# Kernel tuning notes

Hardware: AMD Instinct MI355X
Metric: run time of the kernel (lower is better)

The kernel has to match this reference:

```python
import jax, jax.numpy as jnp
import numpy as np


def _conv1x1(x, w, b):
    # x: (B,Ci,H,W), w: (Co,Ci) -> (B,Co,H,W)
    return jnp.einsum('bchw,oc->bohw', x, w) + b[None, :, None, None]


def _conv3x3(x, w, b):
    # x: (B,Ci,H,W), w: (Co,Ci,3,3), stride 1, padding 1 ('SAME')
    y = jax.lax.conv_general_dilated(
        x, w, window_strides=(1, 1), padding='SAME',
        dimension_numbers=('NCHW', 'OIHW', 'NCHW'))
    return y + b[None, :, None, None]


def setup_inputs() -> dict:
    key = jax.random.key(0)
    ks = jax.random.split(key, 10)
    N, B, Cc, Cf, H, W = 3, 8, 128, 256, 64, 64
    s = 0.05  # weight scale to keep attention logits well-conditioned
    return {
        'contexts': jax.random.normal(ks[0], (N, B, Cc, 2 * H, 2 * W), jnp.float32),
        'mainstream': jax.random.normal(ks[1], (B, Cf, H, W), jnp.float32),
        'Wc_w': jax.random.normal(ks[2], (Cc, Cc), jnp.float32) * s,
        'Wc_b': jax.random.normal(ks[3], (Cc,), jnp.float32) * s,
        'Wf_w': jax.random.normal(ks[4], (Cc, Cf), jnp.float32) * s,
        'Wf_b': jax.random.normal(ks[5], (Cc,), jnp.float32) * s,
        'Wk_w': jax.random.normal(ks[6], (Cc, Cf), jnp.float32) * s,
        'Wk_b': jax.random.normal(ks[7], (Cc,), jnp.float32) * s,
        'Wv_w': jax.random.normal(ks[8], (Cc, Cf, 3, 3), jnp.float32) * s,
        'Wv_b': jax.random.normal(ks[9], (Cc,), jnp.float32) * s,
    }


def reference(contexts, mainstream, Wc_w, Wc_b, Wf_w, Wf_b, Wk_w, Wk_b, Wv_w, Wv_b):
    N, B, Cc = contexts.shape[0], contexts.shape[1], contexts.shape[2]
    H, W = mainstream.shape[2], mainstream.shape[3]

    q = _conv1x1(mainstream, Wf_w, Wf_b)        # (B,Cc,H,W) queries
    mkey = _conv1x1(mainstream, Wk_w, Wk_b)     # (B,Cc,H,W) mainline keys
    vals = _conv3x3(mainstream, Wv_w, Wv_b)     # (B,Cc,H,W) mainline values
    ckeys = jax.vmap(lambda c: _conv1x1(c, Wc_w, Wc_b))(contexts)  # (N,B,Cc,2H,2W)

    # unfold 2x2 sub-pixel blocks: (.., 2H, 2W) -> (.., H, 2, W, 2)
    ckeys = ckeys.reshape(N, B, Cc, H, 2, W, 2)
    cfeat = contexts.reshape(N, B, Cc, H, 2, W, 2)

    # per-pixel cross-attention logits: context keys . query
    logits_ctx = jnp.einsum('nbchiwj,bchw->nbhiwj', ckeys, q)      # (N,B,H,2,W,2)
    # mainline key . query (same logit for all 4 sub-pixels)
    logit_main = jnp.einsum('bchw,bchw->bhw', mkey, q)[None, :, :, None, :, None]
    logits = jnp.concatenate(
        [logits_ctx, jnp.broadcast_to(logit_main, (1, B, H, 2, W, 2))], axis=0)

    attn = jax.nn.softmax(logits, axis=0)                          # (N+1,B,H,2,W,2)

    vfeat = jnp.broadcast_to(vals[None, :, :, :, None, :, None],
                             (1, B, Cc, H, 2, W, 2))
    feats = jnp.concatenate([cfeat, vfeat], axis=0)                # (N+1,B,Cc,H,2,W,2)

    out = jnp.einsum('nbhiwj,nbchiwj->bchiwj', attn, feats)        # (B,Cc,H,2,W,2)
    return out.reshape(B, Cc, 2 * H, 2 * W)
```

## Files before the change

kernel.cpp:

```cpp
#include <hip/hip_runtime.h>

#define NCTX 3
#define B 8
#define CC 128
#define CF 256
#define H 64
#define W 64
#define HW 4096
#define YX 16384

#define WS_BIAS  8388608
#define WS_WALL  8454144
#define WS_MSP   8552960
#define WS_WB    13013504
#define WS_WALLO 13160960

typedef __attribute__((ext_vector_type(8))) short bf16x8;
typedef __attribute__((ext_vector_type(4))) float f32x4;
typedef __attribute__((ext_vector_type(8))) unsigned short u16x8;

__device__ __forceinline__ unsigned short f2b(float f) {
    union { float f; unsigned u; } c; c.f = f;
    unsigned u = c.u + 0x7FFFu + ((c.u >> 16) & 1u);
    return (unsigned short)(u >> 16);
}
__device__ __forceinline__ float b2f(unsigned short u) {
    union { unsigned u; float f; } c; c.u = ((unsigned)u) << 16;
    return c.f;
}

__global__ __launch_bounds__(256) void k0(
    const float* __restrict__ Wc_w, const float* __restrict__ Wc_b,
    const float* __restrict__ Wf_w, const float* __restrict__ Wf_b,
    const float* __restrict__ Wk_w, const float* __restrict__ Wk_b,
    const float* __restrict__ Wv, const float* __restrict__ ms,
    unsigned short* __restrict__ Wall, unsigned short* __restrict__ Wallo,
    float* __restrict__ bias448, unsigned short* __restrict__ Wb,
    unsigned short* __restrict__ msP) {
    __shared__ float Ls[32][65];
    int blk = blockIdx.x;
    int t = threadIdx.x;
    if (blk < 448) {
        int o = blk * 256 + t;
        int ci8 = o & 7;
        int idx = o >> 3;
        int row = idx % 448;
        int sc4 = idx / 448;
        int f = (sc4 >> 2) * 32 + (sc4 & 3) * 8 + ci8;
        float w;
        if (row < 128) {
            float s = 0.f;
            for (int o2 = 0; o2 < 128; ++o2) s += Wc_w[o2 * 128 + row] * Wf_w[o2 * 256 + f];
            w = s;
        } else if (row < 384) {
            int p = (row - 128) >> 1;
            w = (row & 1) ? Wk_w[p * 256 + f] : Wf_w[p * 256 + f];
        } else if (row == 384) {
            float s = 0.f;
            for (int o2 = 0; o2 < 128; ++o2) s += Wc_b[o2] * Wf_w[o2 * 256 + f];
            w = s;
        } else w = 0.f;
        unsigned short hi = f2b(w);
        Wall[o] = hi;
        Wallo[o] = f2b(w - b2f(hi));
        if (o < 448) {
            float bb;
            if (o < 128) {
                float s = 0.f;
                for (int o2 = 0; o2 < 128; ++o2) s += Wc_w[o2 * 128 + o] * Wf_b[o2];
                bb = s;
            } else if (o < 384) {
                int p = (o - 128) >> 1;
                bb = (o & 1) ? Wk_b[p] : Wf_b[p];
            } else if (o == 384) {
                float s = 0.f;
                for (int o2 = 0; o2 < 128; ++o2) s += Wc_b[o2] * Wf_b[o2];
                bb = s;
            } else if (o == 385) bb = -1.f;
            else bb = 0.f;
            bias448[o] = bb;
        }
    } else if (blk < 1600) {
        int o = (blk - 448) * 256 + t;
        int ci8 = o & 7;
        int co  = (o >> 3) & 127;
        int c4  = (o >> 10) & 3;
        int s   = (o >> 12) & 7;
        int khw = o >> 15;
        int ci  = s * 32 + c4 * 8 + ci8;
        int kh  = khw / 3, kw = khw - kh * 3;
        Wb[o] = f2b(Wv[((co * 256 + ci) * 3 + kh) * 3 + kw]);
    } else if (blk < 1860) {
        int i = (blk - 1600) * 256 + t;
        if (i < 66560) {
            size_t off;
            if (i < 33792) {
                int x = i % 66; int r = i / 66;
                int g = r & 31, rowi = (r >> 5) & 1, b = r >> 6;
                off = ((((size_t)b * 66 + rowi * 65) * 32) + g) * 66 + x;
            } else {
                int k = i - 33792;
                int xi = k & 1; int g = (k >> 1) & 31; int y1 = (k >> 6) & 63; int b = k >> 12;
                off = ((((size_t)b * 66 + (y1 + 1)) * 32) + g) * 66 + xi * 65;
            }
            *(u16x8*)&msP[off * 8] = (u16x8){0, 0, 0, 0, 0, 0, 0, 0};
        }
    } else {
        int local = blk - 1860;
        int s = local & 7;
        int h = (local >> 3) & 63;
        int b = local >> 9;
        const float* src = ms + ((size_t)b * 256 + s * 32) * HW + h * 64;
        for (int l = t; l < 2048; l += 256) {
            int ci = l >> 6, w = l & 63;
            Ls[ci][w] = src[ci * HW + w];
        }
        __syncthreads();
        int w = t & 63, gi = t >> 6;
        u16x8 vh;
#pragma unroll
        for (int j = 0; j < 8; ++j) vh[j] = f2b(Ls[gi * 8 + j][w]);
        size_t offH = ((((size_t)b * 66 + (h + 1)) * 32) + (s * 4 + gi)) * 66 + (w + 1);
        *(u16x8*)&msP[offH * 8] = vh;
    }
}

__global__ __launch_bounds__(512, 4) void kfull(
    const float* __restrict__ ms, const unsigned short* __restrict__ msP,
    const unsigned short* __restrict__ Wall, const unsigned short* __restrict__ Wallo,
    const float* __restrict__ bias448, const unsigned short* __restrict__ Wb,
    const float* __restrict__ Wv_b, const float* __restrict__ ctx,
    float* __restrict__ out) {
    __shared__ unsigned char smem[64768] __attribute__((aligned(16)));
    unsigned short* qtS16 = (unsigned short*)smem;
    unsigned short* vS16  = (unsigned short*)(smem + 16384);
    float* biasS = (float*)(smem + 58112);
    float* biasB = (float*)(smem + 59904);
    float* logitS = (float*)(smem + 59904);
    float* lmS   = (float*)(smem + 60416);
    float (*part)[128] = (float (*)[128])(smem + 60672);

    int t = threadIdx.x;
    int lane = t & 63, wid = t >> 6;
    int c4l = lane >> 4, lrow = lane & 15;
    int b = blockIdx.x >> 6, h = blockIdx.x & 63;

    {
        auto Bs = (unsigned short (*)[2][4][64][8])(smem + 32768);
        int wm = wid >> 1, wn = wid & 1;
        int xs = t & 63, g4 = t >> 6;
        int c4w = g4 >> 1, sub = g4 & 1;
        const float* msb = ms + ((size_t)b * 256 + g4 * 4) * HW + h * 64 + xs;
        for (int i = t; i < 448; i += 512) biasS[i] = bias448[i];
        if (t < 128) biasB[t] = Wv_b[t];
        if (t < 64) lmS[t] = 0.f;

        f32x4 acc[7][2];
#pragma unroll
        for (int mf = 0; mf < 7; ++mf)
#pragma unroll
            for (int nf = 0; nf < 2; ++nf) acc[mf][nf] = (f32x4){0.f, 0.f, 0.f, 0.f};

        const bf16x8* Whip = (const bf16x8*)Wall;
        const bf16x8* Wlop = (const bf16x8*)Wallo;

#define CVT_WRITE(bufv, F0, F1, F2, F3) do {                                    \
        unsigned short h0 = f2b(F0), h1 = f2b(F1), h2 = f2b(F2), h3 = f2b(F3);  \
        unsigned short q0 = f2b((F0) - b2f(h0)), q1 = f2b((F1) - b2f(h1));      \
        unsigned short q2 = f2b((F2) - b2f(h2)), q3 = f2b((F3) - b2f(h3));      \
        uint2 hw, lw;                                                           \
        hw.x = (unsigned)h0 | ((unsigned)h1 << 16);                             \
        hw.y = (unsigned)h2 | ((unsigned)h3 << 16);                             \
        lw.x = (unsigned)q0 | ((unsigned)q1 << 16);                             \
        lw.y = (unsigned)q2 | ((unsigned)q3 << 16);                             \
        *(uint2*)&Bs[bufv][0][c4w][xs][sub * 4] = hw;                           \
        *(uint2*)&Bs[bufv][1][c4w][xs][sub * 4] = lw;                           \
    } while (0)

        {
            float f0 = msb[0], f1 = msb[HW], f2 = msb[2 * HW], f3 = msb[3 * HW];
            CVT_WRITE(0, f0, f1, f2, f3);
        }
        __syncthreads();

        for (int s = 0; s < 8; ++s) {
            int cur = s & 1;
            float fn0, fn1, fn2, fn3;
            if (s < 7) {
                const float* p = msb + (size_t)(s + 1) * 32 * HW;
                fn0 = p[0]; fn1 = p[HW]; fn2 = p[2 * HW]; fn3 = p[3 * HW];
            }
            bf16x8 bh[2], bl[2];
#pragma unroll
            for (int nf = 0; nf < 2; ++nf) {
                int x = wn * 32 + nf * 16 + lrow;
                bh[nf] = *(const bf16x8*)&Bs[cur][0][c4l][x][0];
                bl[nf] = *(const bf16x8*)&Bs[cur][1][c4l][x][0];
            }
#pragma unroll
            for (int mf = 0; mf < 7; ++mf) {
                size_t widx = (size_t)(s * 4 + c4l) * 448 + wm * 112 + mf * 16 + lrow;
                bf16x8 ah = Whip[widx];
                bf16x8 al = Wlop[widx];
#pragma unroll
                for (int nf = 0; nf < 2; ++nf) {
                    acc[mf][nf] = __builtin_amdgcn_mfma_f32_16x16x32_bf16(ah, bh[nf], acc[mf][nf], 0, 0, 0);
                    acc[mf][nf] = __builtin_amdgcn_mfma_f32_16x16x32_bf16(ah, bl[nf], acc[mf][nf], 0, 0, 0);
                    acc[mf][nf] = __builtin_amdgcn_mfma_f32_16x16x32_bf16(al, bh[nf], acc[mf][nf], 0, 0, 0);
                }
            }
            if (s < 7) CVT_WRITE(cur ^ 1, fn0, fn1, fn2, fn3);
            __syncthreads();
        }
#undef CVT_WRITE

        int px0 = wn * 32;
        float lmp[2] = {0.f, 0.f};
#pragma unroll
        for (int mf = 0; mf < 7; ++mf) {
            int base = wm * 112 + mf * 16;
            int r0 = base + c4l * 4;
            if (base < 128) {
#pragma unroll
                for (int nf = 0; nf < 2; ++nf) {
                    int x = px0 + nf * 16 + lrow;
                    f32x4 v = acc[mf][nf];
#pragma unroll
                    for (int j = 0; j < 4; ++j)
                        qtS16[(r0 + j) * 64 + x] = f2b(v[j] + biasS[r0 + j]);
                }
            } else {
                float b0 = biasS[r0], b1 = biasS[r0 + 1], b2 = biasS[r0 + 2], b3 = biasS[r0 + 3];
#pragma unroll
                for (int nf = 0; nf < 2; ++nf) {
                    f32x4 v = acc[mf][nf];
                    lmp[nf] += (v[0] + b0) * (v[1] + b1) + (v[2] + b2) * (v[3] + b3);
                }
            }
        }
        if (wm != 0) {
#pragma unroll
            for (int nf = 0; nf < 2; ++nf) {
                lmp[nf] += __shfl_xor(lmp[nf], 16);
                lmp[nf] += __shfl_xor(lmp[nf], 32);
            }
            if (c4l == 0) {
#pragma unroll
                for (int nf = 0; nf < 2; ++nf)
                    atomicAdd(&lmS[px0 + nf * 16 + lrow], lmp[nf]);
            }
        }
    }

    {
        auto Bs = (unsigned short (*)[6336])(smem + 32768);
        int wm = wid >> 1, wn = wid & 1;

        f32x4 acc[2][2];
#pragma unroll
        for (int mf = 0; mf < 2; ++mf)
#pragma unroll
            for (int nf = 0; nf < 2; ++nf) acc[mf][nf] = (f32x4){0.f, 0.f, 0.f, 0.f};

        const bf16x8* Wbp = (const bf16x8*)Wb;

#define STAGE2(bufv, sv) do {                                                       \
        for (int iter = 0; iter < 2; ++iter) {                                      \
            int q0 = iter * 512 + (wid << 6);                                       \
            int q = q0 + lane;                                                      \
            if (q < 792) {                                                          \
                int rc = q / 66; int x = q - rc * 66;                               \
                int r = rc >> 2, c4 = rc & 3;                                       \
                int y = h + r;                               \
                const unsigned short* gp = msP +                                    \
                    (((((size_t)b * 66 + y) * 32) + ((sv) * 4 + c4)) * 66 + x) * 8; \
                unsigned short* lp = &Bs[bufv][q0 * 8];                             \
                __builtin_amdgcn_global_load_lds(                                   \
                    (const __attribute__((address_space(1))) void*)gp,              \
                    (__attribute__((address_space(3))) void*)lp, 16, 0, 0);         \
            }                                                                       \
        }                                                                           \
    } while (0)

        STAGE2(0, 0);
        __syncthreads();

        for (int s = 0; s < 8; ++s) {
            int cur = s & 1;
            if (s < 7) STAGE2(cur ^ 1, s + 1);
#pragma unroll
            for (int khw = 0; khw < 9; ++khw) {
                int kh = khw / 3, kw = khw - 3 * (khw / 3);
                bf16x8 a[2];
#pragma unroll
                for (int mf = 0; mf < 2; ++mf)
                    a[mf] = Wbp[((khw * 8 + s) * 4 + c4l) * 128 + wm * 32 + mf * 16 + lrow];
                bf16x8 bf[2];
#pragma unroll
                for (int nf = 0; nf < 2; ++nf) {
                    int chunk = (kh * 4 + c4l) * 66 + wn * 32 + nf * 16 + lrow + kw;
                    bf[nf] = *(const bf16x8*)&Bs[cur][chunk * 8];
                }
#pragma unroll
                for (int mf = 0; mf < 2; ++mf)
#pragma unroll
                    for (int nf = 0; nf < 2; ++nf)
                        acc[mf][nf] = __builtin_amdgcn_mfma_f32_16x16x32_bf16(
                            a[mf], bf[nf], acc[mf][nf], 0, 0, 0);
            }
            __syncthreads();
        }
#undef STAGE2

#pragma unroll
        for (int mf = 0; mf < 2; ++mf) {
            int co0 = wm * 32 + mf * 16 + c4l * 4;
#pragma unroll
            for (int nf = 0; nf < 2; ++nf) {
                int x = wn * 32 + nf * 16 + lrow;
                f32x4 v = acc[mf][nf];
#pragma unroll
                for (int j = 0; j < 4; ++j)
                    vS16[(co0 + j) * 64 + x] = f2b(v[j] + biasB[co0 + j]);
            }
        }
    }

    __syncthreads();
    {
        const unsigned* qtS32 = (const unsigned*)qtS16;
        const unsigned* vS32  = (const unsigned*)vS16;
        int xg = t & 31, cq = t >> 5;
        int wv = t >> 6;
        unsigned qp[8], vp[8];
#pragma unroll
        for (int j = 0; j < 8; ++j) {
            qp[j] = qtS32[(cq * 8 + j) * 32 + xg];
            vp[j] = vS32[(cq * 8 + j) * 32 + xg];
        }
        float lmx0 = lmS[xg * 2], lmx1 = lmS[xg * 2 + 1];

        for (int yi = 0; yi < 2; ++yi) {
            int y = 2 * h + yi;
            float m[4] = {lmx0, lmx0, lmx1, lmx1};
            float sum[4] = {1.f, 1.f, 1.f, 1.f};
            float4 oa[8];
#pragma unroll
            for (int j = 0; j < 8; ++j) {
                float vx = b2f((unsigned short)(vp[j] & 0xffffu));
                float vy = b2f((unsigned short)(vp[j] >> 16));
                oa[j] = (float4){vx, vx, vy, vy};
            }
#pragma unroll 1
            for (int n = 0; n < 3; ++n) {
                const float* cb = ctx + ((size_t)(n * 8 + b) * 128 + cq * 8) * YX
                                  + (size_t)y * 128 + xg * 4;
                float lp[4] = {0.f, 0.f, 0.f, 0.f};
#pragma unroll
                for (int j = 0; j < 8; ++j) {
                    float4 c = *(const float4*)&cb[(size_t)j * YX];
                    float qx = b2f((unsigned short)(qp[j] & 0xffffu));
                    float qy = b2f((unsigned short)(qp[j] >> 16));
                    lp[0] += c.x * qx;
                    lp[1] += c.y * qx;
                    lp[2] += c.z * qy;
                    lp[3] += c.w * qy;
                }
#pragma unroll
                for (int xl = 0; xl < 4; ++xl) lp[xl] += __shfl_xor(lp[xl], 32);
                __syncthreads();
                if (lane < 32) {
#pragma unroll
                    for (int xl = 0; xl < 4; ++xl) part[wv][xg * 4 + xl] = lp[xl];
                }
                __syncthreads();
                if (t < 128) {
                    float s = 0.f;
#pragma unroll
                    for (int w = 0; w < 8; ++w) s += part[w][t];
                    logitS[t] = s;
                }
                __syncthreads();
                float f[4], e[4];
#pragma unroll
                for (int xl = 0; xl < 4; ++xl) {
                    float ln = logitS[xg * 4 + xl];
                    float nm = fmaxf(m[xl], ln);
                    f[xl] = __expf(m[xl] - nm);
                    e[xl] = __expf(ln - nm);
                    sum[xl] = sum[xl] * f[xl] + e[xl];
                    m[xl] = nm;
                }
#pragma unroll
                for (int j = 0; j < 8; ++j) {
                    float4 c = *(const float4*)&cb[(size_t)j * YX];
                    oa[j].x = oa[j].x * f[0] + e[0] * c.x;
                    oa[j].y = oa[j].y * f[1] + e[1] * c.y;
                    oa[j].z = oa[j].z * f[2] + e[2] * c.z;
                    oa[j].w = oa[j].w * f[3] + e[3] * c.w;
                }
            }
            float r0 = 1.f / sum[0], r1 = 1.f / sum[1], r2 = 1.f / sum[2], r3 = 1.f / sum[3];
            float* obase = out + ((size_t)b * 128 + cq * 8) * YX + (size_t)y * 128 + xg * 4;
#pragma unroll
            for (int j = 0; j < 8; ++j) {
                float4 o;
                o.x = oa[j].x * r0;
                o.y = oa[j].y * r1;
                o.z = oa[j].z * r2;
                o.w = oa[j].w * r3;
                *(float4*)&obase[(size_t)j * YX] = o;
            }
        }
    }
}

extern "C" void kernel_launch(void* const* d_in, const int* in_sizes, int n_in,
                              void* d_out, int out_size, void* d_ws, size_t ws_size,
                              hipStream_t stream) {
    const float* ctx  = (const float*)d_in[0];
    const float* ms   = (const float*)d_in[1];
    const float* Wc_w = (const float*)d_in[2];
    const float* Wc_b = (const float*)d_in[3];
    const float* Wf_w = (const float*)d_in[4];
    const float* Wf_b = (const float*)d_in[5];
    const float* Wk_w = (const float*)d_in[6];
    const float* Wk_b = (const float*)d_in[7];
    const float* Wv_w = (const float*)d_in[8];
    const float* Wv_b = (const float*)d_in[9];
    float* out = (float*)d_out;
    float* ws = (float*)d_ws;
    float* bias448 = ws + WS_BIAS;
    unsigned short* Wallp  = (unsigned short*)(ws + WS_WALL);
    unsigned short* Wallop = (unsigned short*)(ws + WS_WALLO);
    unsigned short* msPp   = (unsigned short*)(ws + WS_MSP);
    unsigned short* Wbp    = (unsigned short*)(ws + WS_WB);

    hipLaunchKernelGGL(k0, dim3(5956), dim3(256), 0, stream, Wc_w, Wc_b, Wf_w, Wf_b,
                       Wk_w, Wk_b, Wv_w, ms, Wallp, Wallop, bias448, Wbp, msPp);
    hipLaunchKernelGGL(kfull, dim3(512), dim3(512), 0, stream, ms, msPp, Wallp, Wallop,
                       bias448, Wbp, Wv_b, ctx, out);
}
```

Measured before the change: 136.8 us.

## Batch context logit reductions across all contexts to cut block barriers

Computes the logits for all three contexts first, then reduces them through shared memory in a single pass, replacing the per-context online softmax with its three barriers per context. The normalized softmax is then applied in a second pass over the context data. This takes barriers per row from nine to two and exposes more independent loads. In exchange each context tile is loaded from global memory twice, once for the logits and once for the weighted sum, and the bigger partial-sum buffer now reuses earlier shared memory regions.

```diff
diff --git a/kernel.cpp b/kernel.cpp
--- a/kernel.cpp
+++ b/kernel.cpp
@@ -136,9 +136,9 @@
     unsigned short* vS16  = (unsigned short*)(smem + 16384);
     float* biasS = (float*)(smem + 58112);
     float* biasB = (float*)(smem + 59904);
-    float* logitS = (float*)(smem + 59904);
     float* lmS   = (float*)(smem + 60416);
-    float (*part)[128] = (float (*)[128])(smem + 60672);
+    float (*partA)[3][128] = (float (*)[3][128])(smem + 32768);
+    float* logitAll = (float*)(smem + 45056);
 
     int t = threadIdx.x;
     int lane = t & 63, wid = t >> 6;
@@ -342,75 +342,82 @@
 
         for (int yi = 0; yi < 2; ++yi) {
             int y = 2 * h + yi;
-            float m[4] = {lmx0, lmx0, lmx1, lmx1};
-            float sum[4] = {1.f, 1.f, 1.f, 1.f};
-            float4 oa[8];
-#pragma unroll
-            for (int j = 0; j < 8; ++j) {
-                float vx = b2f((unsigned short)(vp[j] & 0xffffu));
-                float vy = b2f((unsigned short)(vp[j] >> 16));
-                oa[j] = (float4){vx, vx, vy, vy};
-            }
-#pragma unroll 1
+            const float* cbase = ctx + ((size_t)b * 128 + cq * 8) * YX
+                                 + (size_t)y * 128 + xg * 4;
+            float lp[3][4];
+#pragma unroll
             for (int n = 0; n < 3; ++n) {
-                const float* cb = ctx + ((size_t)(n * 8 + b) * 128 + cq * 8) * YX
-                                  + (size_t)y * 128 + xg * 4;
-                float lp[4] = {0.f, 0.f, 0.f, 0.f};
+                const float* cb = cbase + (size_t)n * 8 * 128 * YX;
+                float l0 = 0.f, l1 = 0.f, l2 = 0.f, l3 = 0.f;
 #pragma unroll
                 for (int j = 0; j < 8; ++j) {
                     float4 c = *(const float4*)&cb[(size_t)j * YX];
                     float qx = b2f((unsigned short)(qp[j] & 0xffffu));
                     float qy = b2f((unsigned short)(qp[j] >> 16));
-                    lp[0] += c.x * qx;
-                    lp[1] += c.y * qx;
-                    lp[2] += c.z * qy;
-                    lp[3] += c.w * qy;
-                }
-#pragma unroll
-                for (int xl = 0; xl < 4; ++xl) lp[xl] += __shfl_xor(lp[xl], 32);
-                __syncthreads();
-                if (lane < 32) {
-#pragma unroll
-                    for (int xl = 0; xl < 4; ++xl) part[wv][xg * 4 + xl] = lp[xl];
-                }
-                __syncthreads();
-                if (t < 128) {
-                    float s = 0.f;
-#pragma unroll
-                    for (int w = 0; w < 8; ++w) s += part[w][t];
-                    logitS[t] = s;
-                }
-                __syncthreads();
-                float f[4], e[4];
-#pragma unroll
-                for (int xl = 0; xl < 4; ++xl) {
-                    float ln = logitS[xg * 4 + xl];
-                    float nm = fmaxf(m[xl], ln);
-                    f[xl] = __expf(m[xl] - nm);
-                    e[xl] = __expf(ln - nm);
-                    sum[xl] = sum[xl] * f[xl] + e[xl];
-                    m[xl] = nm;
-                }
+                    l0 += c.x * qx; l1 += c.y * qx; l2 += c.z * qy; l3 += c.w * qy;
+                }
+                lp[n][0] = l0; lp[n][1] = l1; lp[n][2] = l2; lp[n][3] = l3;
+            }
+#pragma unroll
+            for (int n = 0; n < 3; ++n)
+#pragma unroll
+                for (int xl = 0; xl < 4; ++xl)
+                    lp[n][xl] += __shfl_xor(lp[n][xl], 32);
+            if (lane < 32) {
+#pragma unroll
+                for (int n = 0; n < 3; ++n)
+#pragma unroll
+                    for (int xl = 0; xl < 4; ++xl)
+                        partA[wv][n][xg * 4 + xl] = lp[n][xl];
+            }
+            __syncthreads();
+            if (t < 384) {
+                int n = t >> 7, x = t & 127;
+                float s = 0.f;
+#pragma unroll
+                for (int w = 0; w < 8; ++w) s += partA[w][n][x];
+                logitAll[n * 128 + x] = s;
+            }
+            __syncthreads();
+            float a0[4], a1[4], a2[4], am[4];
+#pragma unroll
+            for (int xl = 0; xl < 4; ++xl) {
+                int x = xg * 4 + xl;
+                float l0 = logitAll[x], l1 = logitAll[128 + x], l2 = logitAll[256 + x];
+                float l3 = (xl < 2) ? lmx0 : lmx1;
+                float mm = fmaxf(fmaxf(l0, l1), fmaxf(l2, l3));
+                float e0 = __expf(l0 - mm), e1 = __expf(l1 - mm);
+                float e2 = __expf(l2 - mm), e3 = __expf(l3 - mm);
+                float inv = 1.f / (e0 + e1 + e2 + e3);
+                a0[xl] = e0 * inv; a1[xl] = e1 * inv; a2[xl] = e2 * inv; am[xl] = e3 * inv;
+            }
+            float4 oa[8];
+#pragma unroll
+            for (int j = 0; j < 8; ++j) {
+                float vx = b2f((unsigned short)(vp[j] & 0xffffu));
+                float vy = b2f((unsigned short)(vp[j] >> 16));
+                oa[j] = (float4){am[0] * vx, am[1] * vx, am[2] * vy, am[3] * vy};
+            }
+#pragma unroll 1
+            for (int n = 0; n < 3; ++n) {
+                const float* cb = cbase + (size_t)n * 8 * 128 * YX;
+                float w0 = (n == 0) ? a0[0] : (n == 1) ? a1[0] : a2[0];
+                float w1 = (n == 0) ? a0[1] : (n == 1) ? a1[1] : a2[1];
+                float w2 = (n == 0) ? a0[2] : (n == 1) ? a1[2] : a2[2];
+                float w3 = (n == 0) ? a0[3] : (n == 1) ? a1[3] : a2[3];
 #pragma unroll
                 for (int j = 0; j < 8; ++j) {
                     float4 c = *(const float4*)&cb[(size_t)j * YX];
-                    oa[j].x = oa[j].x * f[0] + e[0] * c.x;
-                    oa[j].y = oa[j].y * f[1] + e[1] * c.y;
-                    oa[j].z = oa[j].z * f[2] + e[2] * c.z;
-                    oa[j].w = oa[j].w * f[3] + e[3] * c.w;
-                }
-            }
-            float r0 = 1.f / sum[0], r1 = 1.f / sum[1], r2 = 1.f / sum[2], r3 = 1.f / sum[3];
+                    oa[j].x += w0 * c.x;
+                    oa[j].y += w1 * c.y;
+                    oa[j].z += w2 * c.z;
+                    oa[j].w += w3 * c.w;
+                }
+            }
             float* obase = out + ((size_t)b * 128 + cq * 8) * YX + (size_t)y * 128 + xg * 4;
 #pragma unroll
-            for (int j = 0; j < 8; ++j) {
-                float4 o;
-                o.x = oa[j].x * r0;
-                o.y = oa[j].y * r1;
-                o.z = oa[j].z * r2;
-                o.w = oa[j].w * r3;
-                *(float4*)&obase[(size_t)j * YX] = o;
-            }
+            for (int j = 0; j < 8; ++j)
+                *(float4*)&obase[(size_t)j * YX] = oa[j];
         }
     }
 }
```

New measurement: 142.2 us. +3.9%, slower.

## Remap attention phase so each wavefront owns pixels and reduces channels via shuffles

Applied to the files above, without the earlier changes.

The attention phase now assigns each wavefront 16 output columns, with its 64 lanes split into 16 channel groups by 4 pixel groups. The channel reduction for the logits is then done entirely with cross-lane shuffles, removing the shared-memory partial-sum buffer and three block-wide barriers per context. The q/v tiles in shared memory are XOR-swizzled to avoid bank conflicts under the new access pattern. The trade-off is that global context reads become 64-byte runs per channel row instead of 512-byte runs, which may hurt coalescing, and q/v values are re-read from LDS inside the loops.

```diff
diff --git a/kernel.cpp b/kernel.cpp
--- a/kernel.cpp
+++ b/kernel.cpp
@@ -14,6 +14,8 @@
 #define WS_MSP   8552960
 #define WS_WB    13013504
 #define WS_WALLO 13160960
+
+#define SWZ(c, x) ((x) ^ ((((c) >> 3) & 7) << 3))
 
 typedef __attribute__((ext_vector_type(8))) short bf16x8;
 typedef __attribute__((ext_vector_type(4))) float f32x4;
@@ -136,9 +138,7 @@
     unsigned short* vS16  = (unsigned short*)(smem + 16384);
     float* biasS = (float*)(smem + 58112);
     float* biasB = (float*)(smem + 59904);
-    float* logitS = (float*)(smem + 59904);
     float* lmS   = (float*)(smem + 60416);
-    float (*part)[128] = (float (*)[128])(smem + 60672);
 
     int t = threadIdx.x;
     int lane = t & 63, wid = t >> 6;
@@ -224,10 +224,11 @@
 #pragma unroll
                 for (int nf = 0; nf < 2; ++nf) {
                     int x = px0 + nf * 16 + lrow;
+                    int sw = SWZ(r0, x);
                     f32x4 v = acc[mf][nf];
 #pragma unroll
                     for (int j = 0; j < 4; ++j)
-                        qtS16[(r0 + j) * 64 + x] = f2b(v[j] + biasS[r0 + j]);
+                        qtS16[(r0 + j) * 64 + sw] = f2b(v[j] + biasS[r0 + j]);
                 }
             } else {
                 float b0 = biasS[r0], b1 = biasS[r0 + 1], b2 = biasS[r0 + 2], b3 = biasS[r0 + 3];
@@ -318,10 +319,11 @@
 #pragma unroll
             for (int nf = 0; nf < 2; ++nf) {
                 int x = wn * 32 + nf * 16 + lrow;
+                int sw = SWZ(co0, x);
                 f32x4 v = acc[mf][nf];
 #pragma unroll
                 for (int j = 0; j < 4; ++j)
-                    vS16[(co0 + j) * 64 + x] = f2b(v[j] + biasB[co0 + j]);
+                    vS16[(co0 + j) * 64 + sw] = f2b(v[j] + biasB[co0 + j]);
             }
         }
     }
@@ -330,86 +332,75 @@
     {
         const unsigned* qtS32 = (const unsigned*)qtS16;
         const unsigned* vS32  = (const unsigned*)vS16;
-        int xg = t & 31, cq = t >> 5;
-        int wv = t >> 6;
-        unsigned qp[8], vp[8];
-#pragma unroll
-        for (int j = 0; j < 8; ++j) {
-            qp[j] = qtS32[(cq * 8 + j) * 32 + xg];
-            vp[j] = vS32[(cq * 8 + j) * 32 + xg];
-        }
-        float lmx0 = lmS[xg * 2], lmx1 = lmS[xg * 2 + 1];
+        int xg = lane & 3, cq = lane >> 2;
+        int x0 = wid * 16 + xg * 4;
+        int px0 = x0 >> 1;
+        float lm0 = lmS[px0], lm1 = lmS[px0 + 1];
 
         for (int yi = 0; yi < 2; ++yi) {
             int y = 2 * h + yi;
-            float m[4] = {lmx0, lmx0, lmx1, lmx1};
+            float m[4] = {lm0, lm0, lm1, lm1};
             float sum[4] = {1.f, 1.f, 1.f, 1.f};
             float4 oa[8];
 #pragma unroll
             for (int j = 0; j < 8; ++j) {
-                float vx = b2f((unsigned short)(vp[j] & 0xffffu));
-                float vy = b2f((unsigned short)(vp[j] >> 16));
-                oa[j] = (float4){vx, vx, vy, vy};
+                int c = cq * 8 + j;
+                unsigned vv = vS32[(c * 64 + SWZ(c, px0)) >> 1];
+                float v0 = b2f((unsigned short)(vv & 0xffffu));
+                float v1 = b2f((unsigned short)(vv >> 16));
+                oa[j] = (float4){v0, v0, v1, v1};
             }
 #pragma unroll 1
             for (int n = 0; n < 3; ++n) {
                 const float* cb = ctx + ((size_t)(n * 8 + b) * 128 + cq * 8) * YX
-                                  + (size_t)y * 128 + xg * 4;
+                                  + (size_t)y * 128 + x0;
                 float lp[4] = {0.f, 0.f, 0.f, 0.f};
 #pragma unroll
                 for (int j = 0; j < 8; ++j) {
-                    float4 c = *(const float4*)&cb[(size_t)j * YX];
-                    float qx = b2f((unsigned short)(qp[j] & 0xffffu));
-                    float qy = b2f((unsigned short)(qp[j] >> 16));
-                    lp[0] += c.x * qx;
-                    lp[1] += c.y * qx;
-                    lp[2] += c.z * qy;
-                    lp[3] += c.w * qy;
-                }
-#pragma unroll
-                for (int xl = 0; xl < 4; ++xl) lp[xl] += __shfl_xor(lp[xl], 32);
-                __syncthreads();
-                if (lane < 32) {
-#pragma unroll
-                    for (int xl = 0; xl < 4; ++xl) part[wv][xg * 4 + xl] = lp[xl];
-                }
-                __syncthreads();
-                if (t < 128) {
-                    float s = 0.f;
-#pragma unroll
-                    for (int w = 0; w < 8; ++w) s += part[w][t];
-                    logitS[t] = s;
-                }
-                __syncthreads();
+                    float4 c4 = *(const float4*)&cb[(size_t)j * YX];
+                    int c = cq * 8 + j;
+                    unsigned qq = qtS32[(c * 64 + SWZ(c, px0)) >> 1];
+                    float q0 = b2f((unsigned short)(qq & 0xffffu));
+                    float q1 = b2f((unsigned short)(qq >> 16));
+                    lp[0] += c4.x * q0; lp[1] += c4.y * q0;
+                    lp[2] += c4.z * q1; lp[3] += c4.w * q1;
+                }
+#pragma unroll
+                for (int xl = 0; xl < 4; ++xl) {
+                    lp[xl] += __shfl_xor(lp[xl], 4);
+                    lp[xl] += __shfl_xor(lp[xl], 8);
+                    lp[xl] += __shfl_xor(lp[xl], 16);
+                    lp[xl] += __shfl_xor(lp[xl], 32);
+                }
                 float f[4], e[4];
 #pragma unroll
                 for (int xl = 0; xl < 4; ++xl) {
-                    float ln = logitS[xg * 4 + xl];
-                    float nm = fmaxf(m[xl], ln);
+                    float nm = fmaxf(m[xl], lp[xl]);
                     f[xl] = __expf(m[xl] - nm);
-                    e[xl] = __expf(ln - nm);
+                    e[xl] = __expf(lp[xl] - nm);
                     sum[xl] = sum[xl] * f[xl] + e[xl];
                     m[xl] = nm;
                 }
 #pragma unroll
                 for (int j = 0; j < 8; ++j) {
-                    float4 c = *(const float4*)&cb[(size_t)j * YX];
-                    oa[j].x = oa[j].x * f[0] + e[0] * c.x;
-                    oa[j].y = oa[j].y * f[1] + e[1] * c.y;
-                    oa[j].z = oa[j].z * f[2] + e[2] * c.z;
-                    oa[j].w = oa[j].w * f[3] + e[3] * c.w;
-                }
-            }
-            float r0 = 1.f / sum[0], r1 = 1.f / sum[1], r2 = 1.f / sum[2], r3 = 1.f / sum[3];
-            float* obase = out + ((size_t)b * 128 + cq * 8) * YX + (size_t)y * 128 + xg * 4;
+                    float4 c4 = *(const float4*)&cb[(size_t)j * YX];
+                    oa[j].x = oa[j].x * f[0] + e[0] * c4.x;
+                    oa[j].y = oa[j].y * f[1] + e[1] * c4.y;
+                    oa[j].z = oa[j].z * f[2] + e[2] * c4.z;
+                    oa[j].w = oa[j].w * f[3] + e[3] * c4.w;
+                }
+            }
+            float r0i = 1.f / sum[0], r1i = 1.f / sum[1];
+            float r2i = 1.f / sum[2], r3i = 1.f / sum[3];
+            float* ob = out + ((size_t)b * 128 + cq * 8) * YX + (size_t)y * 128 + x0;
 #pragma unroll
             for (int j = 0; j < 8; ++j) {
                 float4 o;
-                o.x = oa[j].x * r0;
-                o.y = oa[j].y * r1;
-                o.z = oa[j].z * r2;
-                o.w = oa[j].w * r3;
-                *(float4*)&obase[(size_t)j * YX] = o;
+                o.x = oa[j].x * r0i;
+                o.y = oa[j].y * r1i;
+                o.z = oa[j].z * r2i;
+                o.w = oa[j].w * r3i;
+                *(float4*)&ob[(size_t)j * YX] = o;
             }
         }
     }
```

After: 151.8 us. +10.9%, slower.
